# Performance work log

Measured on AMD Instinct MI355X. Metric: run time of the kernel, lower is better.

## Reference

```python
import jax, jax.numpy as jnp
import numpy as np

SCALE = 8      # scale_factor from map_to_mat_info
PATCH = 32     # up_delta - low_delta + 1 == right_delta - left_delta + 1 (uniform interior patches)


def setup_inputs() -> dict:
    key = jax.random.key(0)
    mat_h, mat_w = 160, 160
    H = (mat_h - 1) * SCALE + PATCH  # 1304: deltas (0,31,0,31) -> no border clipping
    W = (mat_w - 1) * SCALE + PATCH
    x = jax.random.normal(key, (1, 3, H, W), dtype=jnp.float32)
    rgb_weight = jnp.array([0.299, 0.587, 0.114], dtype=jnp.float32).reshape(1, 3, 1, 1)
    return {"x": x, "rgb_weight": rgb_weight, "mat_h": mat_h, "mat_w": mat_w}


def reference(x, rgb_weight, mat_h, mat_w):
    P = PATCH
    # RGB -> grayscale (convert_gray branch for in_channels == 3)
    gray = jnp.sum(x * rgb_weight, axis=1)[0]  # (H, W)
    # Gather all overlapping PxP patches at stride SCALE -> (mat_h, mat_w, P, P)
    rows = (jnp.arange(mat_h) * SCALE)[:, None] + jnp.arange(P)[None, :]  # (mat_h, P)
    cols = (jnp.arange(mat_w) * SCALE)[:, None] + jnp.arange(P)[None, :]  # (mat_w, P)
    p = gray[rows.reshape(-1)].reshape(mat_h, P, -1)              # (mat_h, P, W)
    p = p[:, :, cols.reshape(-1)].reshape(mat_h, P, mat_w, P)     # (mat_h, P, mat_w, P)
    patches = jnp.transpose(p, (0, 2, 1, 3))                      # (mat_h, mat_w, P, P)
    # torch.rfft(signal_ndim=2, onesided=False) == full 2D FFT; power = re^2 + im^2
    F = jnp.fft.fft2(patches)
    log_power = jnp.log(F.real * F.real + F.imag * F.imag + 1.0)
    # High-frequency region sums (h == w == P, static)
    lo = P // 2 - P // 4 - 1   # 7
    up = P // 2 + P // 4       # 24
    r1 = jnp.sum(log_power[..., lo:up + 1, :], axis=(-2, -1))
    r2 = jnp.sum(log_power[..., up + 1:, lo:up + 1], axis=(-2, -1))
    r3 = jnp.sum(log_power[..., :lo, lo:up + 1], axis=(-2, -1))
    mat = (r1 + r2 + r3)[None, None]  # (1, 1, mat_h, mat_w)
    return mat / jnp.max(mat)
```

## Files before the change

### kernel.cpp

```cpp
#include <hip/hip_runtime.h>
#include <math.h>

#define SCALE 8
#define PSZ 32

__device__ constexpr float C32[16] = {
     1.000000000000000f,  0.980785280403230f,  0.923879532511287f,  0.831469612302545f,
     0.707106781186548f,  0.555570233019602f,  0.382683432365090f,  0.195090322016128f,
     0.000000000000000f, -0.195090322016128f, -0.382683432365090f, -0.555570233019602f,
    -0.707106781186548f, -0.831469612302545f, -0.923879532511287f, -0.980785280403230f };
__device__ constexpr float S32[16] = {
     0.000000000000000f,  0.195090322016128f,  0.382683432365090f,  0.555570233019602f,
     0.707106781186548f,  0.831469612302545f,  0.923879532511287f,  0.980785280403230f,
     1.000000000000000f,  0.980785280403230f,  0.923879532511287f,  0.831469612302545f,
     0.707106781186548f,  0.555570233019602f,  0.382683432365090f,  0.195090322016128f };

__device__ __forceinline__ constexpr int brev4(int i) {
    return ((i & 1) << 3) | ((i & 2) << 1) | ((i & 4) >> 1) | ((i & 8) >> 3);
}

__device__ __forceinline__ void fft16(float re[16], float im[16]) {
#pragma unroll
    for (int i = 0; i < 16; ++i) {
        const int j = brev4(i);
        if (j > i) {
            float t = re[i]; re[i] = re[j]; re[j] = t;
            t = im[i]; im[i] = im[j]; im[j] = t;
        }
    }
#pragma unroll
    for (int s = 1; s <= 4; ++s) {
        const int m = 1 << s;
        const int h = m >> 1;
        const int tstep = 32 >> s;
#pragma unroll
        for (int k = 0; k < 16; k += m) {
#pragma unroll
            for (int j = 0; j < h; ++j) {
                const float wr = C32[j * tstep];
                const float wi = -S32[j * tstep];
                const int a = k + j;
                const int b = k + j + h;
                const float tr = wr * re[b] - wi * im[b];
                const float ti = wr * im[b] + wi * re[b];
                re[b] = re[a] - tr; im[b] = im[a] - ti;
                re[a] = re[a] + tr; im[a] = im[a] + ti;
            }
        }
    }
}

__device__ __forceinline__ unsigned pack_bf2(float hi, float lo) {
    const unsigned uh = __float_as_uint(hi) + 0x8000u;
    const unsigned ul = __float_as_uint(lo) + 0x8000u;
    return (uh & 0xFFFF0000u) | (ul >> 16);
}
__device__ __forceinline__ float bf_hi(unsigned u) { return __uint_as_float(u & 0xFFFF0000u); }
__device__ __forceinline__ float bf_lo(unsigned u) { return __uint_as_float(u << 16); }

__global__ __launch_bounds__(256) void gray_kernel(
        const float* __restrict__ x, const float* __restrict__ w,
        float* __restrict__ g, int n4, long long HW) {
    const int i = blockIdx.x * 256 + threadIdx.x;
    if (i >= n4) return;
    const float w0 = w[0], w1 = w[1], w2 = w[2];
    const float4 a = reinterpret_cast<const float4*>(x)[i];
    const float4 b = reinterpret_cast<const float4*>(x + HW)[i];
    const float4 c = reinterpret_cast<const float4*>(x + 2 * HW)[i];
    float4 o;
    o.x = w0 * a.x + w1 * b.x + w2 * c.x;
    o.y = w0 * a.y + w1 * b.y + w2 * c.y;
    o.z = w0 * a.z + w1 * b.z + w2 * c.z;
    o.w = w0 * a.w + w1 * b.w + w2 * c.w;
    reinterpret_cast<float4*>(g)[i] = o;
}

__global__ __launch_bounds__(256) void hfdft_tile_kernel(
        const float* __restrict__ x, const float* __restrict__ w,
        float* __restrict__ out, float* __restrict__ partial,
        int W, int mat_w, long long HW) {
    __shared__ unsigned spec[2 * 88 * 17];
    __shared__ float red[16];

    const int tid = threadIdx.x;
    const int row0 = blockIdx.y * 64;
    const int col0 = blockIdx.x * 16;

    const bool is_even = (tid < 88);
    const bool is_odd = (tid >= 128 && tid < 216);
    if (is_even || is_odd) {
        const int y = is_even ? tid : (tid - 128);
        const float* base = x + (size_t)(row0 + y) * W + col0;
        const float4* a4 = reinterpret_cast<const float4*>(base);
        const float4* b4 = reinterpret_cast<const float4*>(base + HW);
        const float4* c4 = reinterpret_cast<const float4*>(base + 2 * HW);
        const float w0 = w[0], w1 = w[1], w2 = w[2];

        float win[40];
#pragma unroll
        for (int q = 0; q < 10; ++q) {
            const float4 a = a4[q], b = b4[q], c = c4[q];
            win[4 * q + 0] = w0 * a.x + w1 * b.x + w2 * c.x;
            win[4 * q + 1] = w0 * a.y + w1 * b.y + w2 * c.y;
            win[4 * q + 2] = w0 * a.z + w1 * b.z + w2 * c.z;
            win[4 * q + 3] = w0 * a.w + w1 * b.w + w2 * c.w;
        }

        unsigned* sA = spec + y * 17;
        unsigned* sB = spec + 88 * 17 + y * 17;

        float fr[16], fi[16];
        if (is_even) {
#pragma unroll
            for (int i = 0; i < 16; ++i) {
                fr[i] = win[i] + win[i + 16];
                fi[i] = win[i + 8] + win[i + 24];
            }
            fft16(fr, fi);
            sA[0] = pack_bf2(fr[0], fr[8]);
            sB[0] = pack_bf2(fi[0], fi[8]);
#pragma unroll
            for (int k2 = 1; k2 <= 7; ++k2) {
                const int e2 = 16 - k2;
                const float far_ = 0.5f * (fr[k2] + fr[e2]);
                const float fai_ = 0.5f * (fi[k2] - fi[e2]);
                const float fbr_ = 0.5f * (fi[k2] + fi[e2]);
                const float fbi_ = 0.5f * (fr[e2] - fr[k2]);
                sA[2 * k2] = pack_bf2(far_, fai_);
                sB[2 * k2] = pack_bf2(fbr_, fbi_);
            }
        } else {
#pragma unroll
            for (int i = 0; i < 16; ++i) {
                const float dre = win[i] - win[i + 16];
                const float dim = win[i + 8] - win[i + 24];
                fr[i] = dre * C32[i] + dim * S32[i];
                fi[i] = dim * C32[i] - dre * S32[i];
            }
            fft16(fr, fi);
#pragma unroll
            for (int k2 = 0; k2 <= 7; ++k2) {
                const int o2 = 15 - k2;
                const float far_ = 0.5f * (fr[k2] + fr[o2]);
                const float fai_ = 0.5f * (fi[k2] - fi[o2]);
                const float fbr_ = 0.5f * (fi[k2] + fi[o2]);
                const float fbi_ = 0.5f * (fr[o2] - fr[k2]);
                sA[2 * k2 + 1] = pack_bf2(far_, fai_);
                sB[2 * k2 + 1] = pack_bf2(fbr_, fbi_);
            }
        }
    }

    __syncthreads();

    {
        const int pl = tid >> 4;
        const int slot = tid & 15;
        const int ph = pl >> 1, strip = pl & 1;
        const unsigned* cbp = spec + strip * (88 * 17) + (ph * 8) * 17 + slot;
        const float b1f = (slot >= 7) ? 1.0f : 0.0f;
        const float m1f = (slot >= 8) ? 1.0f : 0.0f;

        float s0 = 0.0f, s1 = 0.0f;

        {
            float er[16], ei[16];
#pragma unroll
            for (int i = 0; i < 16; ++i) {
                const unsigned u0 = cbp[i * 17], u1 = cbp[(i + 16) * 17];
                er[i] = bf_hi(u0) + bf_hi(u1);
                ei[i] = bf_lo(u0) + bf_lo(u1);
            }
            fft16(er, ei);
            if (slot == 0) {
#pragma unroll
                for (int k2 = 0; k2 <= 8; ++k2) {
                    const int kr = 2 * k2;
                    const int b = (k2 == 0) ? 0 : 16 - k2;
                    const float g0r = 0.5f * (er[k2] + er[b]);
                    const float g0i = 0.5f * (ei[k2] - ei[b]);
                    const float g1r = 0.5f * (ei[k2] + ei[b]);
                    const float g1i = 0.5f * (er[b] - er[k2]);
                    const float w0c = (kr >= 7 ? 1.0f : 0.0f) + ((kr >= 8 && kr <= 15) ? 1.0f : 0.0f);
                    const float w16c = 1.0f + ((kr >= 1 && kr <= 15) ? 1.0f : 0.0f);
                    if (w0c > 0.0f)
                        s0 = fmaf(w0c, __logf(g0r * g0r + g0i * g0i + 1.0f), s0);
                    s1 = fmaf(w16c, __logf(g1r * g1r + g1i * g1i + 1.0f), s1);
                }
            } else {
#pragma unroll
                for (int k2 = 0; k2 < 16; ++k2) {
                    const int kr = 2 * k2;
                    const float lp = __logf(er[k2] * er[k2] + ei[k2] * ei[k2] + 1.0f);
                    const float wgt = (kr >= 8 && kr <= 24) ? 2.0f : (b1f + m1f);
                    if (k2 & 1) s1 = fmaf(wgt, lp, s1);
                    else        s0 = fmaf(wgt, lp, s0);
                }
            }
        }

        asm volatile("" ::: "memory");

        {
            float orr[16], oi[16];
#pragma unroll
            for (int i = 0; i < 16; ++i) {
                const unsigned u0 = cbp[i * 17], u1 = cbp[(i + 16) * 17];
                const float dre = bf_hi(u0) - bf_hi(u1);
                const float dim = bf_lo(u0) - bf_lo(u1);
                orr[i] = dre * C32[i] + dim * S32[i];
                oi[i]  = dim * C32[i] - dre * S32[i];
            }
            fft16(orr, oi);
            if (slot == 0) {
#pragma unroll
                for (int k2 = 0; k2 <= 7; ++k2) {
                    const int kr = 2 * k2 + 1;
                    const int b = 15 - k2;
                    const float g0r = 0.5f * (orr[k2] + orr[b]);
                    const float g0i = 0.5f * (oi[k2] - oi[b]);
                    const float g1r = 0.5f * (oi[k2] + oi[b]);
                    const float g1i = 0.5f * (orr[b] - orr[k2]);
                    const float w0c = (kr >= 7 ? 1.0f : 0.0f) + ((kr >= 8 && kr <= 15) ? 1.0f : 0.0f);
                    const float w16c = 2.0f;
                    if (w0c > 0.0f)
                        s0 = fmaf(w0c, __logf(g0r * g0r + g0i * g0i + 1.0f), s0);
                    s1 = fmaf(w16c, __logf(g1r * g1r + g1i * g1i + 1.0f), s1);
                }
            } else {
#pragma unroll
                for (int k2 = 0; k2 < 16; ++k2) {
                    const int kr = 2 * k2 + 1;
                    const float lp = __logf(orr[k2] * orr[k2] + oi[k2] * oi[k2] + 1.0f);
                    float wgt;
                    if (kr == 7)                   wgt = 1.0f + m1f;
                    else if (kr == 25)             wgt = b1f + 1.0f;
                    else if (kr >= 9 && kr <= 23)  wgt = 2.0f;
                    else                           wgt = b1f + m1f;
                    if (k2 & 1) s1 = fmaf(wgt, lp, s1);
                    else        s0 = fmaf(wgt, lp, s0);
                }
            }
        }

        float s = s0 + s1;
#pragma unroll
        for (int off = 8; off >= 1; off >>= 1) s += __shfl_xor(s, off, 16);
        if (slot == 0) {
            out[(blockIdx.y * 8 + ph) * mat_w + blockIdx.x * 2 + strip] = s;
            red[pl] = s;
        }
    }

    __syncthreads();

    if (tid == 0) {
        float m = red[0];
#pragma unroll
        for (int i = 1; i < 16; ++i) m = fmaxf(m, red[i]);
        partial[blockIdx.y * gridDim.x + blockIdx.x] = m;
    }
}

template <bool GRAY_PRE>
__global__ __launch_bounds__(128) void hfdft_patch_kernel(
        const float* __restrict__ x, const float* __restrict__ w,
        float* __restrict__ out, int H, int W, int mat_h, int mat_w) {
    __shared__ unsigned cb[4 * 528];
    __shared__ float red[8];

    const int tid = threadIdx.x;
    const int h = tid >> 6;
    const int lane = tid & 63;
    const int total = mat_h * mat_w;
    const long long HW = (long long)H * W;
    const int Pbase = blockIdx.x * 4;

    {
        const int g = lane >> 5, r = lane & 31;
        int pA = Pbase + 2 * g;
        if (pA > total - 1) pA = total - 1;
        int pB = pA + 1; if (pB > total - 1) pB = total - 1;
        const int phA = pA / mat_w, pwA = pA % mat_w;
        const int phB = pB / mat_w, pwB = pB % mat_w;
        const bool adj = (phA == phB) && (pwB == pwA + 1);
        const int baseA = (phA * SCALE + r) * W + pwA * SCALE;
        const int baseB = (phB * SCALE + r) * W + pwB * SCALE;

        float ar[32], br[32];
        if (GRAY_PRE && adj) {
            float win[40];
            const float4* g4 = reinterpret_cast<const float4*>(x + baseA);
#pragma unroll
            for (int q = 0; q < 10; ++q) {
                const float4 v = g4[q];
                win[4 * q + 0] = v.x; win[4 * q + 1] = v.y;
                win[4 * q + 2] = v.z; win[4 * q + 3] = v.w;
            }
#pragma unroll
            for (int i = 0; i < 32; ++i) { ar[i] = win[i]; br[i] = win[i + 8]; }
        } else if (GRAY_PRE) {
#pragma unroll
            for (int i = 0; i < 32; ++i) { ar[i] = x[baseA + i]; br[i] = x[baseB + i]; }
        } else {
            const float w0 = w[0], w1 = w[1], w2 = w[2];
#pragma unroll
            for (int i = 0; i < 32; ++i) {
                ar[i] = w0 * x[baseA + i] + w1 * x[HW + baseA + i] + w2 * x[2 * HW + baseA + i];
                br[i] = w0 * x[baseB + i] + w1 * x[HW + baseB + i] + w2 * x[2 * HW + baseB + i];
            }
        }

        float fr[16], fi[16];
        if (h == 0) {
#pragma unroll
            for (int i = 0; i < 16; ++i) {
                fr[i] = ar[i] + ar[i + 16];
                fi[i] = br[i] + br[i + 16];
            }
        } else {
#pragma unroll
            for (int i = 0; i < 16; ++i) {
                const float dre = ar[i] - ar[i + 16];
                const float dim = br[i] - br[i + 16];
                fr[i] = dre * C32[i] + dim * S32[i];
                fi[i] = dim * C32[i] - dre * S32[i];
            }
        }

        fft16(fr, fi);

        unsigned* cbA = cb + (2 * g) * 528;
        unsigned* cbB = cbA + 528;
        if (h == 0) {
            cbA[r] = pack_bf2(fr[0], fr[8]);
            cbB[r] = pack_bf2(fi[0], fi[8]);
#pragma unroll
            for (int k2 = 1; k2 <= 7; ++k2) {
                const int e2 = 16 - k2;
                const float far_ = 0.5f * (fr[k2] + fr[e2]);
                const float fai_ = 0.5f * (fi[k2] - fi[e2]);
                const float fbr_ = 0.5f * (fi[k2] + fi[e2]);
                const float fbi_ = 0.5f * (fr[e2] - fr[k2]);
                cbA[(2 * k2) * 33 + r] = pack_bf2(far_, fai_);
                cbB[(2 * k2) * 33 + r] = pack_bf2(fbr_, fbi_);
            }
        } else {
#pragma unroll
            for (int k2 = 0; k2 <= 7; ++k2) {
                const int o2 = 15 - k2;
                const float far_ = 0.5f * (fr[k2] + fr[o2]);
                const float fai_ = 0.5f * (fi[k2] - fi[o2]);
                const float fbr_ = 0.5f * (fi[k2] + fi[o2]);
                const float fbi_ = 0.5f * (fr[o2] - fr[k2]);
                cbA[(2 * k2 + 1) * 33 + r] = pack_bf2(far_, fai_);
                cbB[(2 * k2 + 1) * 33 + r] = pack_bf2(fbr_, fbi_);
            }
        }
    }

    __syncthreads();

    {
        const int pl = lane >> 4, slot = lane & 15;
        int p = Pbase + pl;
        if (p > total - 1) p = total - 1;
        const unsigned* cbp = cb + pl * 528 + slot * 33;

        float fr[16], fi[16];
        if (h == 0) {
#pragma unroll
            for (int i = 0; i < 16; ++i) {
                const unsigned u0 = cbp[i], u1 = cbp[i + 16];
                fr[i] = bf_hi(u0) + bf_hi(u1);
                fi[i] = bf_lo(u0) + bf_lo(u1);
            }
        } else {
#pragma unroll
            for (int i = 0; i < 16; ++i) {
                const unsigned u0 = cbp[i], u1 = cbp[i + 16];
                const float dre = bf_hi(u0) - bf_hi(u1);
                const float dim = bf_lo(u0) - bf_lo(u1);
                fr[i] = dre * C32[i] + dim * S32[i];
                fi[i] = dim * C32[i] - dre * S32[i];
            }
        }

        fft16(fr, fi);

        float s0 = 0.0f, s1 = 0.0f;
        if (slot == 0) {
            if (h == 0) {
#pragma unroll
                for (int k2 = 0; k2 <= 8; ++k2) {
                    const int kr = 2 * k2;
                    const int b = (k2 == 0) ? 0 : 16 - k2;
                    const float g0r = 0.5f * (fr[k2] + fr[b]);
                    const float g0i = 0.5f * (fi[k2] - fi[b]);
                    const float g1r = 0.5f * (fi[k2] + fi[b]);
                    const float g1i = 0.5f * (fr[b] - fr[k2]);
                    const float w0c = (kr >= 7 ? 1.0f : 0.0f) + ((kr >= 8 && kr <= 15) ? 1.0f : 0.0f);
                    const float w16c = 1.0f + ((kr >= 1 && kr <= 15) ? 1.0f : 0.0f);
                    if (w0c > 0.0f)
                        s0 = fmaf(w0c, __logf(g0r * g0r + g0i * g0i + 1.0f), s0);
                    s1 = fmaf(w16c, __logf(g1r * g1r + g1i * g1i + 1.0f), s1);
                }
            } else {
#pragma unroll
                for (int k2 = 0; k2 <= 7; ++k2) {
                    const int kr = 2 * k2 + 1;
                    const int b = 15 - k2;
                    const float g0r = 0.5f * (fr[k2] + fr[b]);
                    const float g0i = 0.5f * (fi[k2] - fi[b]);
                    const float g1r = 0.5f * (fi[k2] + fi[b]);
                    const float g1i = 0.5f * (fr[b] - fr[k2]);
                    const float w0c = (kr >= 7 ? 1.0f : 0.0f) + ((kr >= 8 && kr <= 15) ? 1.0f : 0.0f);
                    const float w16c = 2.0f;
                    if (w0c > 0.0f)
                        s0 = fmaf(w0c, __logf(g0r * g0r + g0i * g0i + 1.0f), s0);
                    s1 = fmaf(w16c, __logf(g1r * g1r + g1i * g1i + 1.0f), s1);
                }
            }
        } else {
            const float b1f = (slot >= 7) ? 1.0f : 0.0f;
            const float m1f = (slot >= 8) ? 1.0f : 0.0f;
            if (h == 0) {
#pragma unroll
                for (int k2 = 0; k2 < 16; ++k2) {
                    const int kr = 2 * k2;
                    const float lp = __logf(fr[k2] * fr[k2] + fi[k2] * fi[k2] + 1.0f);
                    const float wgt = (kr >= 8 && kr <= 24) ? 2.0f : (b1f + m1f);
                    if (k2 & 1) s1 = fmaf(wgt, lp, s1);
                    else        s0 = fmaf(wgt, lp, s0);
                }
            } else {
#pragma unroll
                for (int k2 = 0; k2 < 16; ++k2) {
                    const int kr = 2 * k2 + 1;
                    const float lp = __logf(fr[k2] * fr[k2] + fi[k2] * fi[k2] + 1.0f);
                    float wgt;
                    if (kr == 7)                   wgt = 1.0f + m1f;
                    else if (kr == 25)             wgt = b1f + 1.0f;
                    else if (kr >= 9 && kr <= 23)  wgt = 2.0f;
                    else                           wgt = b1f + m1f;
                    if (k2 & 1) s1 = fmaf(wgt, lp, s1);
                    else        s0 = fmaf(wgt, lp, s0);
                }
            }
        }

        float s = s0 + s1;
#pragma unroll
        for (int off = 8; off >= 1; off >>= 1) s += __shfl_xor(s, off, 16);
        if (slot == 0) red[pl * 2 + h] = s;
    }

    __syncthreads();

    if (tid < 4) {
        const int p = Pbase + tid;
        if (p < total) out[p] = red[tid * 2] + red[tid * 2 + 1];
    }
}

__global__ __launch_bounds__(1024) void max_kernel(
        const float* __restrict__ sums, int n, float* __restrict__ partial) {
    __shared__ float sm[16];
    float m = 0.0f;
    for (int i = blockIdx.x * 1024 + threadIdx.x; i < n; i += gridDim.x * 1024)
        m = fmaxf(m, sums[i]);
#pragma unroll
    for (int off = 32; off >= 1; off >>= 1) m = fmaxf(m, __shfl_xor(m, off, 64));
    if ((threadIdx.x & 63) == 0) sm[threadIdx.x >> 6] = m;
    __syncthreads();
    if (threadIdx.x == 0) {
#pragma unroll
        for (int i = 1; i < 16; ++i) m = fmaxf(m, sm[i]);
        partial[blockIdx.x] = m;
    }
}

__global__ __launch_bounds__(256) void norm_kernel(
        float* __restrict__ out, int n,
        const float* __restrict__ partial, int np) {
    __shared__ float sm[4];
    float m = 0.0f;
    for (int i = threadIdx.x; i < np; i += 256) m = fmaxf(m, partial[i]);
#pragma unroll
    for (int off = 32; off >= 1; off >>= 1) m = fmaxf(m, __shfl_xor(m, off, 64));
    if ((threadIdx.x & 63) == 0) sm[threadIdx.x >> 6] = m;
    __syncthreads();
    m = fmaxf(fmaxf(sm[0], sm[1]), fmaxf(sm[2], sm[3]));
    const int i = blockIdx.x * 256 + threadIdx.x;
    if (i < n) out[i] = out[i] / m;
}

extern "C" void kernel_launch(void* const* d_in, const int* in_sizes, int n_in,
                              void* d_out, int out_size, void* d_ws, size_t ws_size,
                              hipStream_t stream) {
    const float* x = (const float*)d_in[0];
    const float* w = (const float*)d_in[1];
    float* out = (float*)d_out;

    const int HWi = in_sizes[0] / 3;
    const int H = (int)(sqrt((double)HWi) + 0.5);
    const int W = H;
    const long long HW = (long long)H * W;
    const int mat = (int)(sqrt((double)out_size) + 0.5);
    const int total = mat * mat;

    float* partial = (float*)d_ws;
    float* gray = (float*)((char*)d_ws + 8192);
    const int nparts = (mat / 2) * (mat / 8);

    const bool shape_ok = ((mat & 7) == 0) && (W == (mat - 1) * SCALE + PSZ)
                          && (H == W) && ((W & 3) == 0)
                          && ws_size >= (size_t)nparts * 4;

    if (shape_ok) {
        dim3 gridT(mat / 2, mat / 8);
        hipLaunchKernelGGL(hfdft_tile_kernel, gridT, dim3(256), 0, stream,
                           x, w, out, partial, W, mat, HW);
        hipLaunchKernelGGL(norm_kernel, dim3((total + 255) / 256), dim3(256), 0, stream,
                           out, total, partial, nparts);
    } else if (ws_size >= 8192 + (size_t)HW * 4 && (W & 3) == 0) {
        const int n4 = (int)(HW / 4);
        hipLaunchKernelGGL(gray_kernel, dim3((n4 + 255) / 256), dim3(256), 0, stream,
                           x, w, gray, n4, HW);
        hipLaunchKernelGGL((hfdft_patch_kernel<true>), dim3((total + 3) / 4), dim3(128), 0, stream,
                           gray, w, out, H, W, mat, mat);
        hipLaunchKernelGGL(max_kernel, dim3(8), dim3(1024), 0, stream, out, total, partial);
        hipLaunchKernelGGL(norm_kernel, dim3((total + 255) / 256), dim3(256), 0, stream,
                           out, total, partial, 8);
    } else {
        hipLaunchKernelGGL((hfdft_patch_kernel<false>), dim3((total + 3) / 4), dim3(128), 0, stream,
                           x, w, out, H, W, mat, mat);
        hipLaunchKernelGGL(max_kernel, dim3(8), dim3(1024), 0, stream, out, total, partial);
        hipLaunchKernelGGL(norm_kernel, dim3((total + 255) / 256), dim3(256), 0, stream,
                           out, total, partial, 8);
    }
}
```

Baseline: 45.01 us.

## Precompute grayscale in separate pass and transpose LDS spectrum layout for vector reads

```diff
diff --git a/kernel.cpp b/kernel.cpp
--- a/kernel.cpp
+++ b/kernel.cpp
@@ -3,6 +3,9 @@
 
 #define SCALE 8
 #define PSZ 32
+
+#define RSTRIDE 92
+#define SSTRIDE (17 * RSTRIDE)
 
 __device__ constexpr float C32[16] = {
      1.000000000000000f,  0.980785280403230f,  0.923879532511287f,  0.831469612302545f,
@@ -76,10 +79,9 @@
 }
 
 __global__ __launch_bounds__(256) void hfdft_tile_kernel(
-        const float* __restrict__ x, const float* __restrict__ w,
-        float* __restrict__ out, float* __restrict__ partial,
-        int W, int mat_w, long long HW) {
-    __shared__ unsigned spec[2 * 88 * 17];
+        const float* __restrict__ g, float* __restrict__ out,
+        float* __restrict__ partial, int W, int mat_w) {
+    __shared__ unsigned spec[2 * SSTRIDE];
     __shared__ float red[16];
 
     const int tid = threadIdx.x;
@@ -90,24 +92,18 @@
     const bool is_odd = (tid >= 128 && tid < 216);
     if (is_even || is_odd) {
         const int y = is_even ? tid : (tid - 128);
-        const float* base = x + (size_t)(row0 + y) * W + col0;
-        const float4* a4 = reinterpret_cast<const float4*>(base);
-        const float4* b4 = reinterpret_cast<const float4*>(base + HW);
-        const float4* c4 = reinterpret_cast<const float4*>(base + 2 * HW);
-        const float w0 = w[0], w1 = w[1], w2 = w[2];
-
+        const float4* g4 = reinterpret_cast<const float4*>(
+            g + (size_t)(row0 + y) * W + col0);
         float win[40];
 #pragma unroll
         for (int q = 0; q < 10; ++q) {
-            const float4 a = a4[q], b = b4[q], c = c4[q];
-            win[4 * q + 0] = w0 * a.x + w1 * b.x + w2 * c.x;
-            win[4 * q + 1] = w0 * a.y + w1 * b.y + w2 * c.y;
-            win[4 * q + 2] = w0 * a.z + w1 * b.z + w2 * c.z;
-            win[4 * q + 3] = w0 * a.w + w1 * b.w + w2 * c.w;
-        }
-
-        unsigned* sA = spec + y * 17;
-        unsigned* sB = spec + 88 * 17 + y * 17;
+            const float4 v = g4[q];
+            win[4 * q + 0] = v.x; win[4 * q + 1] = v.y;
+            win[4 * q + 2] = v.z; win[4 * q + 3] = v.w;
+        }
+
+        unsigned* sA = spec + y;
+        unsigned* sB = spec + SSTRIDE + y;
 
         float fr[16], fi[16];
         if (is_even) {
@@ -126,8 +122,8 @@
                 const float fai_ = 0.5f * (fi[k2] - fi[e2]);
                 const float fbr_ = 0.5f * (fi[k2] + fi[e2]);
                 const float fbi_ = 0.5f * (fr[e2] - fr[k2]);
-                sA[2 * k2] = pack_bf2(far_, fai_);
-                sB[2 * k2] = pack_bf2(fbr_, fbi_);
+                sA[(2 * k2) * RSTRIDE] = pack_bf2(far_, fai_);
+                sB[(2 * k2) * RSTRIDE] = pack_bf2(fbr_, fbi_);
             }
         } else {
 #pragma unroll
@@ -145,8 +141,8 @@
                 const float fai_ = 0.5f * (fi[k2] - fi[o2]);
                 const float fbr_ = 0.5f * (fi[k2] + fi[o2]);
                 const float fbi_ = 0.5f * (fr[o2] - fr[k2]);
-                sA[2 * k2 + 1] = pack_bf2(far_, fai_);
-                sB[2 * k2 + 1] = pack_bf2(fbr_, fbi_);
+                sA[(2 * k2 + 1) * RSTRIDE] = pack_bf2(far_, fai_);
+                sB[(2 * k2 + 1) * RSTRIDE] = pack_bf2(fbr_, fbi_);
             }
         }
     }
@@ -157,19 +153,29 @@
         const int pl = tid >> 4;
         const int slot = tid & 15;
         const int ph = pl >> 1, strip = pl & 1;
-        const unsigned* cbp = spec + strip * (88 * 17) + (ph * 8) * 17 + slot;
         const float b1f = (slot >= 7) ? 1.0f : 0.0f;
         const float m1f = (slot >= 8) ? 1.0f : 0.0f;
 
+        unsigned u[32];
+        {
+            const uint4* p4 = reinterpret_cast<const uint4*>(
+                spec + strip * SSTRIDE + slot * RSTRIDE + ph * 8);
+#pragma unroll
+            for (int q = 0; q < 8; ++q) {
+                const uint4 v = p4[q];
+                u[4 * q + 0] = v.x; u[4 * q + 1] = v.y;
+                u[4 * q + 2] = v.z; u[4 * q + 3] = v.w;
+            }
+        }
+
         float s0 = 0.0f, s1 = 0.0f;
 
         {
             float er[16], ei[16];
 #pragma unroll
             for (int i = 0; i < 16; ++i) {
-                const unsigned u0 = cbp[i * 17], u1 = cbp[(i + 16) * 17];
-                er[i] = bf_hi(u0) + bf_hi(u1);
-                ei[i] = bf_lo(u0) + bf_lo(u1);
+                er[i] = bf_hi(u[i]) + bf_hi(u[i + 16]);
+                ei[i] = bf_lo(u[i]) + bf_lo(u[i + 16]);
             }
             fft16(er, ei);
             if (slot == 0) {
@@ -199,15 +205,12 @@
             }
         }
 
-        asm volatile("" ::: "memory");
-
         {
             float orr[16], oi[16];
 #pragma unroll
             for (int i = 0; i < 16; ++i) {
-                const unsigned u0 = cbp[i * 17], u1 = cbp[(i + 16) * 17];
-                const float dre = bf_hi(u0) - bf_hi(u1);
-                const float dim = bf_lo(u0) - bf_lo(u1);
+                const float dre = bf_hi(u[i]) - bf_hi(u[i + 16]);
+                const float dim = bf_lo(u[i]) - bf_lo(u[i + 16]);
                 orr[i] = dre * C32[i] + dim * S32[i];
                 oi[i]  = dim * C32[i] - dre * S32[i];
             }
@@ -512,18 +515,22 @@
     float* partial = (float*)d_ws;
     float* gray = (float*)((char*)d_ws + 8192);
     const int nparts = (mat / 2) * (mat / 8);
+    const size_t need = 8192 + (size_t)HW * 4;
 
     const bool shape_ok = ((mat & 7) == 0) && (W == (mat - 1) * SCALE + PSZ)
                           && (H == W) && ((W & 3) == 0)
-                          && ws_size >= (size_t)nparts * 4;
+                          && ws_size >= need && (size_t)nparts * 4 <= 8192;
 
     if (shape_ok) {
+        const int n4 = (int)(HW / 4);
+        hipLaunchKernelGGL(gray_kernel, dim3((n4 + 255) / 256), dim3(256), 0, stream,
+                           x, w, gray, n4, HW);
         dim3 gridT(mat / 2, mat / 8);
         hipLaunchKernelGGL(hfdft_tile_kernel, gridT, dim3(256), 0, stream,
-                           x, w, out, partial, W, mat, HW);
+                           gray, out, partial, W, mat);
         hipLaunchKernelGGL(norm_kernel, dim3((total + 255) / 256), dim3(256), 0, stream,
                            out, total, partial, nparts);
-    } else if (ws_size >= 8192 + (size_t)HW * 4 && (W & 3) == 0) {
+    } else if (ws_size >= need && (W & 3) == 0) {
         const int n4 = (int)(HW / 4);
         hipLaunchKernelGGL(gray_kernel, dim3((n4 + 255) / 256), dim3(256), 0, stream,
                            x, w, gray, n4, HW);
```

Result: faster. 43.71 us (-2.9%).
